# Kernel optimization log

Measured on AMD Instinct MI355X. Metric: run time of the kernel, lower is better.

The kernel has to match this reference:

```python
import jax, jax.numpy as jnp
import numpy as np

N = 8192        # n_nodes
NFEAT = 512
NHID = 256
AVG_DEG = 32
K = 64          # mean_kwargs k
TEMP = 1.0      # mean_kwargs temperature


def setup_inputs() -> dict:
    key = jax.random.key(0)
    ks = jax.random.split(key, 5)
    x = jax.random.normal(ks[0], (N, NFEAT), jnp.float32)
    edge_index = jax.random.randint(ks[1], (2, N * AVG_DEG), 0, N, dtype=jnp.int64)
    W1 = jax.random.normal(ks[2], (NFEAT, NHID), jnp.float32) / np.sqrt(NFEAT)
    b1 = jnp.zeros((NHID,), jnp.float32)
    W2 = jax.random.normal(ks[3], (NHID, NHID), jnp.float32) / np.sqrt(NHID)
    b2 = jnp.zeros((NHID,), jnp.float32)
    return {"x": x, "edge_index": edge_index, "W1": W1, "b1": b1, "W2": W2, "b2": b2}


def _gcn_norm(edge_index, n, dtype):
    # PyG gcn_norm: add self-loops (weight 1), deg over col, sym normalization
    loops = jnp.arange(n, dtype=edge_index.dtype)
    row = jnp.concatenate([edge_index[0], loops])
    col = jnp.concatenate([edge_index[1], loops])
    w = jnp.ones(row.shape[0], dtype)
    deg = jnp.zeros((n,), dtype).at[col].add(w)
    dis = jnp.where(deg > 0, jax.lax.rsqrt(jnp.where(deg > 0, deg, 1.0)), 0.0)
    return row, col, dis[row] * w * dis[col]


def _soft_k_medoid(row, col, w, x):
    # soft_weighted_medoid_k_neighborhood(A, x, k=K, temperature=TEMP, with_weight_correction=True)
    n, d = x.shape
    A = jnp.zeros((n, n), x.dtype).at[row, col].add(w)   # coalesced dense adjacency
    topk_a, topk_idx = jax.lax.top_k(A, K)               # [n, K] neighbor weights / ids
    xk = x[topk_idx]                                     # [n, K, d]
    sq = jnp.sum(xk * xk, axis=-1)                       # [n, K]
    G = jnp.einsum('nkd,nld->nkl', xk, xk)               # Gram per node
    d2 = jnp.maximum(sq[:, :, None] + sq[:, None, :] - 2.0 * G, 0.0)
    pos = d2 > 0
    dist = jnp.where(pos, jnp.sqrt(jnp.where(pos, d2, 1.0)), 0.0)  # safe sqrt (grad-safe)
    # weighted sum of distances to each top-k candidate j: c[n,j] = sum_l a[n,l] * ||x_l - x_j||
    c = jnp.einsum('nl,nlj->nj', topk_a, dist)
    c = jnp.where(topk_a == 0, jnp.finfo(x.dtype).max, c)
    soft = jax.nn.softmax(-c / TEMP, axis=-1)            # [n, K]
    soft = soft * topk_a                                 # with_weight_correction
    soft = soft / jnp.sum(soft, axis=-1, keepdims=True)
    row_sum = jnp.sum(A, axis=-1)                        # preserve neighborhood mass
    return row_sum[:, None] * jnp.einsum('nk,nkd->nd', soft, xk)


def reference(x, edge_index, W1, b1, W2, b2):
    n = x.shape[0]
    row, col, w = _gcn_norm(edge_index, n, x.dtype)
    h = jax.nn.relu(_soft_k_medoid(row, col, w, x @ W1) + b1)   # gc1 + relu (dropout: eval = identity)
    return jax.nn.relu(_soft_k_medoid(row, col, w, h @ W2) + b2)  # gc2 + relu
```

## Files before the change

kernel.cpp:

```cpp
#include <hip/hip_runtime.h>

typedef _Float16 half4 __attribute__((ext_vector_type(4)));
typedef _Float16 half8 __attribute__((ext_vector_type(8)));
typedef float f32x4 __attribute__((ext_vector_type(4)));

#define NNODE 8192
#define NHID  256
#define RCAP  128
#define KCAP  64

__global__ __launch_bounds__(256) void k_fused1(
    int* deg, int* rowcnt, int* flag, const void* edges,
    const float* __restrict__ W1, _Float16* __restrict__ w1T,
    const float* __restrict__ W2, _Float16* __restrict__ w2T) {
    const int b = blockIdx.x, t = threadIdx.x;
    if (b < 32) {
        int i = b * 256 + t;
        deg[i] = 0; rowcnt[i] = 0;
        if (i == 0) {
            const long long* e = (const long long*)edges;
            int ok = 1;
            for (int k = 0; k < 64; ++k) { long long v = e[k]; if (v < 0 || v >= NNODE) ok = 0; }
            *flag = ok;
        }
    } else if (b < 32 + 512) {
        int idx = (b - 32) * 256 + t;
        int k = idx >> 8, n = idx & 255;
        w1T[(size_t)n * 512 + k] = (_Float16)W1[idx];
    } else {
        int idx = (b - 544) * 256 + t;
        int k = idx >> 8, n = idx & 255;
        w2T[(size_t)n * 256 + k] = (_Float16)W2[idx];
    }
}

#define GLS 72

__device__ __forceinline__ void gemm_body(
    const float* __restrict__ Af32, const _Float16* __restrict__ Ahi,
    const _Float16* __restrict__ BT, _Float16* __restrict__ Chi,
    int K, int af32, int bm, int bn) {
    __shared__ _Float16 sA[64][GLS];
    __shared__ _Float16 sB[64][GLS];
    const int t = threadIdx.x;
    const int lane = t & 63, L15 = lane & 15, q = lane >> 4;
    const int w = t >> 6, wr = w >> 1, wc = w & 1;
    f32x4 acc[2][2];
#pragma unroll
    for (int a = 0; a < 2; ++a)
#pragma unroll
        for (int b2 = 0; b2 < 2; ++b2) acc[a][b2] = (f32x4){0.f, 0.f, 0.f, 0.f};

    for (int k0 = 0; k0 < K; k0 += 64) {
        if (af32) {
#pragma unroll
            for (int i = 0; i < 4; ++i) {
                int row = i * 16 + (t >> 4), kc = (t & 15) * 4;
                float4 v = *(const float4*)(Af32 + (size_t)(bm + row) * K + k0 + kc);
                half4 h;
                h[0] = (_Float16)v.x; h[1] = (_Float16)v.y;
                h[2] = (_Float16)v.z; h[3] = (_Float16)v.w;
                *(half4*)&sA[row][kc] = h;
            }
        } else {
#pragma unroll
            for (int i = 0; i < 2; ++i) {
                int row = i * 32 + (t >> 3), ch = t & 7;
                *(half8*)&sA[row][ch * 8] =
                    *(const half8*)(Ahi + (size_t)(bm + row) * K + k0 + ch * 8);
            }
        }
#pragma unroll
        for (int i = 0; i < 2; ++i) {
            int row = i * 32 + (t >> 3), ch = t & 7;
            *(half8*)&sB[row][ch * 8] =
                *(const half8*)(BT + (size_t)(bn + row) * K + k0 + ch * 8);
        }
        __syncthreads();
#pragma unroll
        for (int ks = 0; ks < 2; ++ks) {
            const int ko = ks * 32 + q * 8;
            half8 ah[2], bh[2];
#pragma unroll
            for (int tr = 0; tr < 2; ++tr)
                ah[tr] = *(const half8*)&sA[32 * wr + 16 * tr + L15][ko];
#pragma unroll
            for (int tc = 0; tc < 2; ++tc)
                bh[tc] = *(const half8*)&sB[32 * wc + 16 * tc + L15][ko];
#pragma unroll
            for (int tr = 0; tr < 2; ++tr)
#pragma unroll
                for (int tc = 0; tc < 2; ++tc)
                    acc[tr][tc] = __builtin_amdgcn_mfma_f32_16x16x32_f16(ah[tr], bh[tc], acc[tr][tc], 0, 0, 0);
        }
        __syncthreads();
    }
#pragma unroll
    for (int tr = 0; tr < 2; ++tr)
#pragma unroll
        for (int tc = 0; tc < 2; ++tc)
#pragma unroll
            for (int r = 0; r < 4; ++r) {
                int rowg = bm + 32 * wr + 16 * tr + q * 4 + r;
                int colg = bn + 32 * wc + 16 * tc + L15;
                Chi[(size_t)rowg * NHID + colg] = (_Float16)acc[tr][tc][r];
            }
}

__global__ __launch_bounds__(256) void k_fused2(
    const void* edges, const int* flag, int* rowcnt, int* nbr, int* deg, int E, int nbuild,
    const float* __restrict__ x, const _Float16* __restrict__ w1T, _Float16* __restrict__ X1) {
    if ((int)blockIdx.x < nbuild) {
        int i = blockIdx.x * 256 + threadIdx.x;
        int total = E + NNODE;
        if (i >= total) return;
        int r, c;
        if (i < E) {
            if (*flag) {
                const long long* e = (const long long*)edges;
                r = (int)e[i]; c = (int)e[E + i];
            } else {
                const int* e = (const int*)edges;
                r = e[i]; c = e[E + i];
            }
        } else { r = i - E; c = r; }
        int pos = atomicAdd(&rowcnt[r], 1);
        if (pos < RCAP) nbr[r * RCAP + pos] = c;
        atomicAdd(&deg[c], 1);
    } else {
        int g = blockIdx.x - nbuild;
        gemm_body(x, nullptr, w1T, X1, 512, 1, (g >> 2) * 64, (g & 3) * 64);
    }
}

__global__ __launch_bounds__(256) void k_gemm(
    const _Float16* __restrict__ Ahi, const _Float16* __restrict__ BT,
    _Float16* __restrict__ Chi, int K) {
    gemm_body(nullptr, Ahi, BT, Chi, K, 0, blockIdx.x * 64, blockIdx.y * 64);
}

__global__ __launch_bounds__(256) void k_dedup(const int* __restrict__ nbr,
                                               const int* __restrict__ rowcnt,
                                               const int* __restrict__ deg,
                                               int* __restrict__ cols,
                                               float* __restrict__ wout,
                                               float* __restrict__ rsum) {
    __shared__ int lc[2][RCAP];
    __shared__ float lw[2][RCAP];
    __shared__ unsigned char kp[2][RCAP];
    __shared__ int s_cw[2][2];
    __shared__ float s_rw[2][2];
    const int t = threadIdx.x;
    const int half = t >> 7, st = t & 127;
    const int wid = st >> 6, lane = t & 63;
    const int r = blockIdx.x * 2 + half;
    int n = rowcnt[r]; if (n > RCAP) n = RCAP;
    if (st < n) lc[half][st] = nbr[r * RCAP + st];
    __syncthreads();
    float dr = 1.f / sqrtf((float)deg[r]);
    bool keep = false; float wv = 0.f;
    if (st < n) {
        int c = lc[half][st];
        int mult = 0; bool first = true;
        for (int i = 0; i < n; ++i) {
            int ci = lc[half][i];
            if (ci == c) { mult++; if (i < st) first = false; }
        }
        keep = first;
        if (first) wv = (float)mult * dr * (1.f / sqrtf((float)deg[c]));
    }
    kp[half][st] = keep ? 1 : 0; lw[half][st] = wv;
    float rv = wv;
#pragma unroll
    for (int d = 1; d < 64; d <<= 1) rv += __shfl_xor(rv, d, 64);
    unsigned long long b = __ballot(keep);
    int pre = __popcll(b & ((1ull << lane) - 1ull));
    int cw = __popcll(b);
    if (lane == 0) { s_cw[half][wid] = cw; s_rw[half][wid] = rv; }
    __syncthreads();
    int total = s_cw[half][0] + s_cw[half][1];
    if (st == 0) rsum[r] = s_rw[half][0] + s_rw[half][1];
    const int base = r * KCAP;
    if (total <= KCAP) {
        int off = (wid ? s_cw[half][0] : 0) + pre;
        if (keep) { cols[base + off] = lc[half][st]; wout[base + off] = wv; }
        for (int m = total + st; m < KCAP; m += 128) { cols[base + m] = r; wout[base + m] = 0.f; }
    } else if (st == 0) {
        for (int s = 0; s < KCAP; ++s) {
            int best = -1;
            for (int i = 0; i < n; ++i) {
                if (!kp[half][i]) continue;
                if (best < 0 || lw[half][i] > lw[half][best] ||
                    (lw[half][i] == lw[half][best] && lc[half][i] < lc[half][best])) best = i;
            }
            cols[base + s] = lc[half][best]; wout[base + s] = lw[half][best]; kp[half][best] = 0;
        }
    }
}

#define MS 264

__global__ __launch_bounds__(256, 4) void k_medoid(
    const _Float16* __restrict__ Xhi,
    const float* __restrict__ bias,
    float* __restrict__ OutF, _Float16* __restrict__ OutHi,
    const int* __restrict__ cols, const float* __restrict__ wts,
    const float* __restrict__ rsum, int writeH) {
    __shared__ _Float16 sh[64][MS];
    __shared__ float s_a[64];
    __shared__ float s_sq[64];
    __shared__ float s_cpart[2][64];
    __shared__ float s_u[64];
    __shared__ int   s_cols[64];
    __shared__ float s_red[4][288];

    const int node = blockIdx.x;
    const int t = threadIdx.x;
    const int w = t >> 6, lane = t & 63;
    const int L15 = lane & 15, q = lane >> 4;
    const int wr = w >> 1, wc = w & 1;

    if (t < 64) { s_cols[t] = cols[node * KCAP + t]; s_a[t] = wts[node * KCAP + t]; }
    __syncthreads();

    {
        const int ch = t & 31, rr = t >> 5;
        float ps[8];
#pragma unroll
        for (int i = 0; i < 8; ++i) {
            int l = i * 8 + rr;
            half8 v = *(const half8*)(Xhi + ((size_t)s_cols[l] << 8) + ch * 8);
            *(half8*)&sh[l][ch * 8] = v;
            float s = 0.f;
#pragma unroll
            for (int e = 0; e < 8; ++e) { float f = (float)v[e]; s = fmaf(f, f, s); }
            ps[i] = s;
        }
#pragma unroll
        for (int d = 1; d < 32; d <<= 1)
#pragma unroll
            for (int i = 0; i < 8; ++i) ps[i] += __shfl_xor(ps[i], d, 64);
        if (ch == 0) {
#pragma unroll
            for (int i = 0; i < 8; ++i) s_sq[i * 8 + rr] = ps[i];
        }
    }
    __syncthreads();

    f32x4 acc[2][2];
#pragma unroll
    for (int a = 0; a < 2; ++a)
#pragma unroll
        for (int b = 0; b < 2; ++b) acc[a][b] = (f32x4){0.f, 0.f, 0.f, 0.f};
#pragma unroll
    for (int ks = 0; ks < 8; ++ks) {
        const int ko = ks * 32 + q * 8;
        half8 ah[2], bh[2];
#pragma unroll
        for (int tr = 0; tr < 2; ++tr) ah[tr] = *(const half8*)&sh[32 * wr + 16 * tr + L15][ko];
#pragma unroll
        for (int tc = 0; tc < 2; ++tc) bh[tc] = *(const half8*)&sh[32 * wc + 16 * tc + L15][ko];
#pragma unroll
        for (int tr = 0; tr < 2; ++tr)
#pragma unroll
            for (int tc = 0; tc < 2; ++tc)
                acc[tr][tc] = __builtin_amdgcn_mfma_f32_16x16x32_f16(ah[tr], bh[tc], acc[tr][tc], 0, 0, 0);
    }

#pragma unroll
    for (int tc = 0; tc < 2; ++tc) {
        const int colg = 32 * wc + 16 * tc + L15;
        const float sqc = s_sq[colg];
        float pj = 0.f;
#pragma unroll
        for (int tr = 0; tr < 2; ++tr)
#pragma unroll
            for (int r = 0; r < 4; ++r) {
                int rowg = 32 * wr + 16 * tr + q * 4 + r;
                float d2 = s_sq[rowg] + sqc - 2.f * acc[tr][tc][r];
                float dist = d2 > 0.f ? __builtin_amdgcn_sqrtf(d2) : 0.f;
                pj = fmaf(s_a[rowg], dist, pj);
            }
        pj += __shfl_xor(pj, 16, 64);
        pj += __shfl_xor(pj, 32, 64);
        if (q == 0) s_cpart[wr][colg] = pj;
    }
    __syncthreads();

    if (w == 0) {
        int j = lane;
        float c = s_cpart[0][j] + s_cpart[1][j];
        float aj = s_a[j];
        bool valid = aj > 0.f;
        float cv = valid ? c : 3.4e38f;
        float mn = cv;
#pragma unroll
        for (int d = 1; d < 64; d <<= 1) mn = fminf(mn, __shfl_xor(mn, d, 64));
        float e = valid ? __expf(mn - c) * aj : 0.f;
        float s = e;
#pragma unroll
        for (int d = 1; d < 64; d <<= 1) s += __shfl_xor(s, d, 64);
        s_u[j] = e * (rsum[node] / s);
    }
    __syncthreads();

    const int oct = t & 31, jb = t >> 5;
    float accd[8] = {0.f, 0.f, 0.f, 0.f, 0.f, 0.f, 0.f, 0.f};
#pragma unroll
    for (int jj = 0; jj < 8; ++jj) {
        int j = jb * 8 + jj;
        float u = s_u[j];
        half8 xv = *(const half8*)&sh[j][8 * oct];
#pragma unroll
        for (int e = 0; e < 8; ++e) accd[e] = fmaf(u, (float)xv[e], accd[e]);
    }
#pragma unroll
    for (int e = 0; e < 8; ++e) accd[e] += __shfl_xor(accd[e], 32, 64);
    if (lane < 32) {
#pragma unroll
        for (int e = 0; e < 8; ++e) s_red[w][9 * oct + e] = accd[e];
    }
    __syncthreads();
    const int idx = 9 * (t >> 3) + (t & 7);
    float o = s_red[0][idx] + s_red[1][idx] + s_red[2][idx] + s_red[3][idx];
    float res = fmaxf(o + bias[t], 0.f);
    size_t oi = (size_t)node * NHID + t;
    if (writeH) OutHi[oi] = (_Float16)res;
    else        OutF[oi] = res;
}

extern "C" void kernel_launch(void* const* d_in, const int* in_sizes, int n_in,
                              void* d_out, int out_size, void* d_ws, size_t ws_size,
                              hipStream_t stream) {
    const float* x  = (const float*)d_in[0];
    const void*  ei = d_in[1];
    const float* W1 = (const float*)d_in[2];
    const float* b1 = (const float*)d_in[3];
    const float* W2 = (const float*)d_in[4];
    const float* b2 = (const float*)d_in[5];
    float* out = (float*)d_out;
    const int E = in_sizes[1] / 2;

    char* p = (char*)d_ws;
    auto alloc = [&](size_t bytes) { char* q = p; p += (bytes + 255) & ~(size_t)255; return q; };
    int*      deg    = (int*)alloc((size_t)NNODE * 4);
    int*      rowcnt = (int*)alloc((size_t)NNODE * 4);
    int*      flag   = (int*)alloc(256);
    int*      colsA  = (int*)alloc((size_t)NNODE * KCAP * 4);
    float*    wA     = (float*)alloc((size_t)NNODE * KCAP * 4);
    float*    rsum   = (float*)alloc((size_t)NNODE * 4);
    _Float16* w1T    = (_Float16*)alloc((size_t)512 * NHID * 2);
    _Float16* w2T    = (_Float16*)alloc((size_t)NHID * NHID * 2);
    _Float16* X1hi   = (_Float16*)alloc((size_t)NNODE * NHID * 2);
    _Float16* Hhi    = (_Float16*)alloc((size_t)NNODE * NHID * 2);
    int*      nbr    = (int*)alloc((size_t)NNODE * RCAP * 4);

    const int nbuild = (E + NNODE + 255) / 256;

    k_fused1<<<32 + 512 + 256, 256, 0, stream>>>(deg, rowcnt, flag, ei, W1, w1T, W2, w2T);
    k_fused2<<<nbuild + 512, 256, 0, stream>>>(ei, flag, rowcnt, nbr, deg, E, nbuild, x, w1T, X1hi);
    k_dedup<<<NNODE / 2, 256, 0, stream>>>(nbr, rowcnt, deg, colsA, wA, rsum);
    k_medoid<<<NNODE, 256, 0, stream>>>(X1hi, b1, nullptr, Hhi, colsA, wA, rsum, 1);
    k_gemm<<<dim3(NNODE / 64, NHID / 64), 256, 0, stream>>>(Hhi, w2T, X1hi, 256);
    k_medoid<<<NNODE, 256, 0, stream>>>(X1hi, b2, out, nullptr, colsA, wA, rsum, 0);
}
```

Baseline: 240.0 us.

## Add half-size medoid path for nodes with at most 32 neighbors

k_dedup now records each row's deduplicated neighbor count. k_medoid uses it to branch: rows with 32 or fewer neighbors gather only 32 feature rows, compute a single 32x32 Gram tile (one MFMA tile per wave), and skip the padded rows in the final weighted sum. Both paths now take squared norms from the Gram diagonal, replacing the separate sum-of-squares shuffle reduction. This cuts gather traffic and MFMA work for the roughly half of nodes below the threshold, at the cost of a divergent, more complex kernel and higher register pressure.

Result: faster. 218.4 us (-9.0%).

```diff
diff --git a/kernel.cpp b/kernel.cpp
--- a/kernel.cpp
+++ b/kernel.cpp
@@ -144,7 +144,8 @@
                                                const int* __restrict__ deg,
                                                int* __restrict__ cols,
                                                float* __restrict__ wout,
-                                               float* __restrict__ rsum) {
+                                               float* __restrict__ rsum,
+                                               int* __restrict__ ncnt) {
     __shared__ int lc[2][RCAP];
     __shared__ float lw[2][RCAP];
     __shared__ unsigned char kp[2][RCAP];
@@ -179,7 +180,7 @@
     if (lane == 0) { s_cw[half][wid] = cw; s_rw[half][wid] = rv; }
     __syncthreads();
     int total = s_cw[half][0] + s_cw[half][1];
-    if (st == 0) rsum[r] = s_rw[half][0] + s_rw[half][1];
+    if (st == 0) { rsum[r] = s_rw[half][0] + s_rw[half][1]; ncnt[r] = total; }
     const int base = r * KCAP;
     if (total <= KCAP) {
         int off = (wid ? s_cw[half][0] : 0) + pre;
@@ -205,7 +206,7 @@
     const float* __restrict__ bias,
     float* __restrict__ OutF, _Float16* __restrict__ OutHi,
     const int* __restrict__ cols, const float* __restrict__ wts,
-    const float* __restrict__ rsum, int writeH) {
+    const float* __restrict__ rsum, const int* __restrict__ ncnt, int writeH) {
     __shared__ _Float16 sh[64][MS];
     __shared__ float s_a[64];
     __shared__ float s_sq[64];
@@ -219,71 +220,110 @@
     const int w = t >> 6, lane = t & 63;
     const int L15 = lane & 15, q = lane >> 4;
     const int wr = w >> 1, wc = w & 1;
+    const bool small = (ncnt[node] <= 32);
 
     if (t < 64) { s_cols[t] = cols[node * KCAP + t]; s_a[t] = wts[node * KCAP + t]; }
     __syncthreads();
 
     {
         const int ch = t & 31, rr = t >> 5;
-        float ps[8];
-#pragma unroll
-        for (int i = 0; i < 8; ++i) {
-            int l = i * 8 + rr;
-            half8 v = *(const half8*)(Xhi + ((size_t)s_cols[l] << 8) + ch * 8);
-            *(half8*)&sh[l][ch * 8] = v;
-            float s = 0.f;
-#pragma unroll
-            for (int e = 0; e < 8; ++e) { float f = (float)v[e]; s = fmaf(f, f, s); }
-            ps[i] = s;
-        }
-#pragma unroll
-        for (int d = 1; d < 32; d <<= 1)
-#pragma unroll
-            for (int i = 0; i < 8; ++i) ps[i] += __shfl_xor(ps[i], d, 64);
-        if (ch == 0) {
-#pragma unroll
-            for (int i = 0; i < 8; ++i) s_sq[i * 8 + rr] = ps[i];
-        }
-    }
-    __syncthreads();
-
-    f32x4 acc[2][2];
-#pragma unroll
-    for (int a = 0; a < 2; ++a)
-#pragma unroll
-        for (int b = 0; b < 2; ++b) acc[a][b] = (f32x4){0.f, 0.f, 0.f, 0.f};
-#pragma unroll
-    for (int ks = 0; ks < 8; ++ks) {
-        const int ko = ks * 32 + q * 8;
-        half8 ah[2], bh[2];
-#pragma unroll
-        for (int tr = 0; tr < 2; ++tr) ah[tr] = *(const half8*)&sh[32 * wr + 16 * tr + L15][ko];
-#pragma unroll
-        for (int tc = 0; tc < 2; ++tc) bh[tc] = *(const half8*)&sh[32 * wc + 16 * tc + L15][ko];
-#pragma unroll
-        for (int tr = 0; tr < 2; ++tr)
-#pragma unroll
-            for (int tc = 0; tc < 2; ++tc)
-                acc[tr][tc] = __builtin_amdgcn_mfma_f32_16x16x32_f16(ah[tr], bh[tc], acc[tr][tc], 0, 0, 0);
-    }
-
-#pragma unroll
-    for (int tc = 0; tc < 2; ++tc) {
-        const int colg = 32 * wc + 16 * tc + L15;
-        const float sqc = s_sq[colg];
+        if (small) {
+#pragma unroll
+            for (int i = 0; i < 4; ++i) {
+                int l = i * 8 + rr;
+                *(half8*)&sh[l][ch * 8] = *(const half8*)(Xhi + ((size_t)s_cols[l] << 8) + ch * 8);
+            }
+        } else {
+#pragma unroll
+            for (int i = 0; i < 8; ++i) {
+                int l = i * 8 + rr;
+                *(half8*)&sh[l][ch * 8] = *(const half8*)(Xhi + ((size_t)s_cols[l] << 8) + ch * 8);
+            }
+        }
+    }
+    __syncthreads();
+
+    if (small) {
+        f32x4 acc = (f32x4){0.f, 0.f, 0.f, 0.f};
+#pragma unroll
+        for (int ks = 0; ks < 8; ++ks) {
+            const int ko = ks * 32 + q * 8;
+            half8 ah = *(const half8*)&sh[16 * wr + L15][ko];
+            half8 bh = *(const half8*)&sh[16 * wc + L15][ko];
+            acc = __builtin_amdgcn_mfma_f32_16x16x32_f16(ah, bh, acc, 0, 0, 0);
+        }
+        if (wr == wc) {
+#pragma unroll
+            for (int r = 0; r < 4; ++r)
+                if (L15 == q * 4 + r) s_sq[16 * wr + L15] = acc[r];
+        }
+        __syncthreads();
+        f32x4 sq4 = *(const f32x4*)&s_sq[16 * wr + 4 * q];
+        f32x4 a4  = *(const f32x4*)&s_a [16 * wr + 4 * q];
+        const float sqc = s_sq[16 * wc + L15];
         float pj = 0.f;
 #pragma unroll
-        for (int tr = 0; tr < 2; ++tr)
-#pragma unroll
-            for (int r = 0; r < 4; ++r) {
-                int rowg = 32 * wr + 16 * tr + q * 4 + r;
-                float d2 = s_sq[rowg] + sqc - 2.f * acc[tr][tc][r];
-                float dist = d2 > 0.f ? __builtin_amdgcn_sqrtf(d2) : 0.f;
-                pj = fmaf(s_a[rowg], dist, pj);
-            }
+        for (int r = 0; r < 4; ++r) {
+            float d2 = sq4[r] + sqc - 2.f * acc[r];
+            float dist = d2 > 0.f ? __builtin_amdgcn_sqrtf(d2) : 0.f;
+            pj = fmaf(a4[r], dist, pj);
+        }
         pj += __shfl_xor(pj, 16, 64);
         pj += __shfl_xor(pj, 32, 64);
-        if (q == 0) s_cpart[wr][colg] = pj;
+        if (q == 0) s_cpart[wr][16 * wc + L15] = pj;
+    } else {
+        f32x4 acc[2][2];
+#pragma unroll
+        for (int a = 0; a < 2; ++a)
+#pragma unroll
+            for (int b = 0; b < 2; ++b) acc[a][b] = (f32x4){0.f, 0.f, 0.f, 0.f};
+#pragma unroll
+        for (int ks = 0; ks < 8; ++ks) {
+            const int ko = ks * 32 + q * 8;
+            half8 ah[2], bh[2];
+#pragma unroll
+            for (int tr = 0; tr < 2; ++tr) ah[tr] = *(const half8*)&sh[32 * wr + 16 * tr + L15][ko];
+#pragma unroll
+            for (int tc = 0; tc < 2; ++tc) bh[tc] = *(const half8*)&sh[32 * wc + 16 * tc + L15][ko];
+#pragma unroll
+            for (int tr = 0; tr < 2; ++tr)
+#pragma unroll
+                for (int tc = 0; tc < 2; ++tc)
+                    acc[tr][tc] = __builtin_amdgcn_mfma_f32_16x16x32_f16(ah[tr], bh[tc], acc[tr][tc], 0, 0, 0);
+        }
+#pragma unroll
+        for (int tr = 0; tr < 2; ++tr)
+#pragma unroll
+            for (int tc = 0; tc < 2; ++tc)
+                if (32 * wr + 16 * tr == 32 * wc + 16 * tc) {
+#pragma unroll
+                    for (int r = 0; r < 4; ++r)
+                        if (L15 == q * 4 + r) s_sq[32 * wr + 16 * tr + L15] = acc[tr][tc][r];
+                }
+        __syncthreads();
+        f32x4 sq4[2], a4[2];
+#pragma unroll
+        for (int tr = 0; tr < 2; ++tr) {
+            sq4[tr] = *(const f32x4*)&s_sq[32 * wr + 16 * tr + 4 * q];
+            a4[tr]  = *(const f32x4*)&s_a [32 * wr + 16 * tr + 4 * q];
+        }
+#pragma unroll
+        for (int tc = 0; tc < 2; ++tc) {
+            const int colg = 32 * wc + 16 * tc + L15;
+            const float sqc = s_sq[colg];
+            float pj = 0.f;
+#pragma unroll
+            for (int tr = 0; tr < 2; ++tr)
+#pragma unroll
+                for (int r = 0; r < 4; ++r) {
+                    float d2 = sq4[tr][r] + sqc - 2.f * acc[tr][tc][r];
+                    float dist = d2 > 0.f ? __builtin_amdgcn_sqrtf(d2) : 0.f;
+                    pj = fmaf(a4[tr][r], dist, pj);
+                }
+            pj += __shfl_xor(pj, 16, 64);
+            pj += __shfl_xor(pj, 32, 64);
+            if (q == 0) s_cpart[wr][colg] = pj;
+        }
     }
     __syncthreads();
 
@@ -306,13 +346,15 @@
 
     const int oct = t & 31, jb = t >> 5;
     float accd[8] = {0.f, 0.f, 0.f, 0.f, 0.f, 0.f, 0.f, 0.f};
-#pragma unroll
-    for (int jj = 0; jj < 8; ++jj) {
-        int j = jb * 8 + jj;
-        float u = s_u[j];
-        half8 xv = *(const half8*)&sh[j][8 * oct];
-#pragma unroll
-        for (int e = 0; e < 8; ++e) accd[e] = fmaf(u, (float)xv[e], accd[e]);
+    if (!small || jb < 4) {
+#pragma unroll
+        for (int jj = 0; jj < 8; ++jj) {
+            int j = jb * 8 + jj;
+            float u = s_u[j];
+            half8 xv = *(const half8*)&sh[j][8 * oct];
+#pragma unroll
+            for (int e = 0; e < 8; ++e) accd[e] = fmaf(u, (float)xv[e], accd[e]);
+        }
     }
 #pragma unroll
     for (int e = 0; e < 8; ++e) accd[e] += __shfl_xor(accd[e], 32, 64);
@@ -349,6 +391,7 @@
     int*      colsA  = (int*)alloc((size_t)NNODE * KCAP * 4);
     float*    wA     = (float*)alloc((size_t)NNODE * KCAP * 4);
     float*    rsum   = (float*)alloc((size_t)NNODE * 4);
+    int*      ncnt   = (int*)alloc((size_t)NNODE * 4);
     _Float16* w1T    = (_Float16*)alloc((size_t)512 * NHID * 2);
     _Float16* w2T    = (_Float16*)alloc((size_t)NHID * NHID * 2);
     _Float16* X1hi   = (_Float16*)alloc((size_t)NNODE * NHID * 2);
@@ -359,8 +402,8 @@
 
     k_fused1<<<32 + 512 + 256, 256, 0, stream>>>(deg, rowcnt, flag, ei, W1, w1T, W2, w2T);
     k_fused2<<<nbuild + 512, 256, 0, stream>>>(ei, flag, rowcnt, nbr, deg, E, nbuild, x, w1T, X1hi);
-    k_dedup<<<NNODE / 2, 256, 0, stream>>>(nbr, rowcnt, deg, colsA, wA, rsum);
-    k_medoid<<<NNODE, 256, 0, stream>>>(X1hi, b1, nullptr, Hhi, colsA, wA, rsum, 1);
+    k_dedup<<<NNODE / 2, 256, 0, stream>>>(nbr, rowcnt, deg, colsA, wA, rsum, ncnt);
+    k_medoid<<<NNODE, 256, 0, stream>>>(X1hi, b1, nullptr, Hhi, colsA, wA, rsum, ncnt, 1);
     k_gemm<<<dim3(NNODE / 64, NHID / 64), 256, 0, stream>>>(Hhi, w2T, X1hi, 256);
-    k_medoid<<<NNODE, 256, 0, stream>>>(X1hi, b2, out, nullptr, colsA, wA, rsum, 0);
-}
+    k_medoid<<<NNODE, 256, 0, stream>>>(X1hi, b2, out, nullptr, colsA, wA, rsum, ncnt, 0);
+}
```

## Halve medoid shared tile via two-phase Gram, precast x to fp16

Applied to the files above, without the earlier changes.

The medoid kernel now stages the 64 gathered neighbor rows in two 128-column halves, so its LDS tile is half the size and launch bounds allow 6 blocks per CU instead of 4. Squared norms are read off the Gram diagonal instead of a separate shuffle reduction. The final weighted sum re-reads the first half of each row from global memory because only the second half is still in LDS. Separately, x is converted to fp16 in a dedicated pass in the first kernel, so the first GEMM loads fp16 tiles directly. This costs an extra global round trip of x and extra gathered reads in the medoid kernel.

Result: faster. 214.6 us (-10.6%).

```diff
diff --git a/kernel.cpp b/kernel.cpp
--- a/kernel.cpp
+++ b/kernel.cpp
@@ -12,7 +12,8 @@
 __global__ __launch_bounds__(256) void k_fused1(
     int* deg, int* rowcnt, int* flag, const void* edges,
     const float* __restrict__ W1, _Float16* __restrict__ w1T,
-    const float* __restrict__ W2, _Float16* __restrict__ w2T) {
+    const float* __restrict__ W2, _Float16* __restrict__ w2T,
+    const float* __restrict__ x, _Float16* __restrict__ xh) {
     const int b = blockIdx.x, t = threadIdx.x;
     if (b < 32) {
         int i = b * 256 + t;
@@ -23,12 +24,19 @@
             for (int k = 0; k < 64; ++k) { long long v = e[k]; if (v < 0 || v >= NNODE) ok = 0; }
             *flag = ok;
         }
-    } else if (b < 32 + 512) {
-        int idx = (b - 32) * 256 + t;
+    } else if (b < 32 + 4096) {
+        int i = (b - 32) * 256 + t;
+        float4 v = ((const float4*)x)[i];
+        half4 h;
+        h[0] = (_Float16)v.x; h[1] = (_Float16)v.y;
+        h[2] = (_Float16)v.z; h[3] = (_Float16)v.w;
+        *(half4*)&xh[4 * (size_t)i] = h;
+    } else if (b < 32 + 4096 + 512) {
+        int idx = (b - 4128) * 256 + t;
         int k = idx >> 8, n = idx & 255;
         w1T[(size_t)n * 512 + k] = (_Float16)W1[idx];
     } else {
-        int idx = (b - 544) * 256 + t;
+        int idx = (b - 4640) * 256 + t;
         int k = idx >> 8, n = idx & 255;
         w2T[(size_t)n * 256 + k] = (_Float16)W2[idx];
     }
@@ -37,9 +45,8 @@
 #define GLS 72
 
 __device__ __forceinline__ void gemm_body(
-    const float* __restrict__ Af32, const _Float16* __restrict__ Ahi,
-    const _Float16* __restrict__ BT, _Float16* __restrict__ Chi,
-    int K, int af32, int bm, int bn) {
+    const _Float16* __restrict__ Ahi, const _Float16* __restrict__ BT,
+    _Float16* __restrict__ Chi, int K, int bm, int bn) {
     __shared__ _Float16 sA[64][GLS];
     __shared__ _Float16 sB[64][GLS];
     const int t = threadIdx.x;
@@ -52,27 +59,11 @@
         for (int b2 = 0; b2 < 2; ++b2) acc[a][b2] = (f32x4){0.f, 0.f, 0.f, 0.f};
 
     for (int k0 = 0; k0 < K; k0 += 64) {
-        if (af32) {
-#pragma unroll
-            for (int i = 0; i < 4; ++i) {
-                int row = i * 16 + (t >> 4), kc = (t & 15) * 4;
-                float4 v = *(const float4*)(Af32 + (size_t)(bm + row) * K + k0 + kc);
-                half4 h;
-                h[0] = (_Float16)v.x; h[1] = (_Float16)v.y;
-                h[2] = (_Float16)v.z; h[3] = (_Float16)v.w;
-                *(half4*)&sA[row][kc] = h;
-            }
-        } else {
-#pragma unroll
-            for (int i = 0; i < 2; ++i) {
-                int row = i * 32 + (t >> 3), ch = t & 7;
-                *(half8*)&sA[row][ch * 8] =
-                    *(const half8*)(Ahi + (size_t)(bm + row) * K + k0 + ch * 8);
-            }
-        }
 #pragma unroll
         for (int i = 0; i < 2; ++i) {
             int row = i * 32 + (t >> 3), ch = t & 7;
+            *(half8*)&sA[row][ch * 8] =
+                *(const half8*)(Ahi + (size_t)(bm + row) * K + k0 + ch * 8);
             *(half8*)&sB[row][ch * 8] =
                 *(const half8*)(BT + (size_t)(bn + row) * K + k0 + ch * 8);
         }
@@ -109,7 +100,7 @@
 
 __global__ __launch_bounds__(256) void k_fused2(
     const void* edges, const int* flag, int* rowcnt, int* nbr, int* deg, int E, int nbuild,
-    const float* __restrict__ x, const _Float16* __restrict__ w1T, _Float16* __restrict__ X1) {
+    const _Float16* __restrict__ xh, const _Float16* __restrict__ w1T, _Float16* __restrict__ X1) {
     if ((int)blockIdx.x < nbuild) {
         int i = blockIdx.x * 256 + threadIdx.x;
         int total = E + NNODE;
@@ -129,14 +120,14 @@
         atomicAdd(&deg[c], 1);
     } else {
         int g = blockIdx.x - nbuild;
-        gemm_body(x, nullptr, w1T, X1, 512, 1, (g >> 2) * 64, (g & 3) * 64);
+        gemm_body(xh, w1T, X1, 512, (g >> 2) * 64, (g & 3) * 64);
     }
 }
 
 __global__ __launch_bounds__(256) void k_gemm(
     const _Float16* __restrict__ Ahi, const _Float16* __restrict__ BT,
     _Float16* __restrict__ Chi, int K) {
-    gemm_body(nullptr, Ahi, BT, Chi, K, 0, blockIdx.x * 64, blockIdx.y * 64);
+    gemm_body(Ahi, BT, Chi, K, blockIdx.x * 64, blockIdx.y * 64);
 }
 
 __global__ __launch_bounds__(256) void k_dedup(const int* __restrict__ nbr,
@@ -198,15 +189,15 @@
     }
 }
 
-#define MS 264
-
-__global__ __launch_bounds__(256, 4) void k_medoid(
+#define SK 136
+
+__global__ __launch_bounds__(256, 6) void k_medoid(
     const _Float16* __restrict__ Xhi,
     const float* __restrict__ bias,
     float* __restrict__ OutF, _Float16* __restrict__ OutHi,
     const int* __restrict__ cols, const float* __restrict__ wts,
     const float* __restrict__ rsum, int writeH) {
-    __shared__ _Float16 sh[64][MS];
+    __shared__ _Float16 sh[64][SK];
     __shared__ float s_a[64];
     __shared__ float s_sq[64];
     __shared__ float s_cpart[2][64];
@@ -223,50 +214,55 @@
     if (t < 64) { s_cols[t] = cols[node * KCAP + t]; s_a[t] = wts[node * KCAP + t]; }
     __syncthreads();
 
-    {
-        const int ch = t & 31, rr = t >> 5;
-        float ps[8];
-#pragma unroll
-        for (int i = 0; i < 8; ++i) {
-            int l = i * 8 + rr;
-            half8 v = *(const half8*)(Xhi + ((size_t)s_cols[l] << 8) + ch * 8);
-            *(half8*)&sh[l][ch * 8] = v;
-            float s = 0.f;
-#pragma unroll
-            for (int e = 0; e < 8; ++e) { float f = (float)v[e]; s = fmaf(f, f, s); }
-            ps[i] = s;
-        }
-#pragma unroll
-        for (int d = 1; d < 32; d <<= 1)
-#pragma unroll
-            for (int i = 0; i < 8; ++i) ps[i] += __shfl_xor(ps[i], d, 64);
-        if (ch == 0) {
-#pragma unroll
-            for (int i = 0; i < 8; ++i) s_sq[i * 8 + rr] = ps[i];
-        }
-    }
-    __syncthreads();
-
     f32x4 acc[2][2];
 #pragma unroll
     for (int a = 0; a < 2; ++a)
 #pragma unroll
         for (int b = 0; b < 2; ++b) acc[a][b] = (f32x4){0.f, 0.f, 0.f, 0.f};
-#pragma unroll
-    for (int ks = 0; ks < 8; ++ks) {
-        const int ko = ks * 32 + q * 8;
-        half8 ah[2], bh[2];
-#pragma unroll
-        for (int tr = 0; tr < 2; ++tr) ah[tr] = *(const half8*)&sh[32 * wr + 16 * tr + L15][ko];
-#pragma unroll
-        for (int tc = 0; tc < 2; ++tc) bh[tc] = *(const half8*)&sh[32 * wc + 16 * tc + L15][ko];
-#pragma unroll
-        for (int tr = 0; tr < 2; ++tr)
-#pragma unroll
-            for (int tc = 0; tc < 2; ++tc)
-                acc[tr][tc] = __builtin_amdgcn_mfma_f32_16x16x32_f16(ah[tr], bh[tc], acc[tr][tc], 0, 0, 0);
-    }
-
+
+    const int ch = t & 15, rr = t >> 4;
+    for (int phase = 0; phase < 2; ++phase) {
+#pragma unroll
+        for (int i = 0; i < 4; ++i) {
+            int l = i * 16 + rr;
+            *(half8*)&sh[l][ch * 8] =
+                *(const half8*)(Xhi + ((size_t)s_cols[l] << 8) + phase * 128 + ch * 8);
+        }
+        __syncthreads();
+#pragma unroll
+        for (int ks = 0; ks < 4; ++ks) {
+            const int ko = ks * 32 + q * 8;
+            half8 ah[2], bh[2];
+#pragma unroll
+            for (int tr = 0; tr < 2; ++tr) ah[tr] = *(const half8*)&sh[32 * wr + 16 * tr + L15][ko];
+#pragma unroll
+            for (int tc = 0; tc < 2; ++tc) bh[tc] = *(const half8*)&sh[32 * wc + 16 * tc + L15][ko];
+#pragma unroll
+            for (int tr = 0; tr < 2; ++tr)
+#pragma unroll
+                for (int tc = 0; tc < 2; ++tc)
+                    acc[tr][tc] = __builtin_amdgcn_mfma_f32_16x16x32_f16(ah[tr], bh[tc], acc[tr][tc], 0, 0, 0);
+        }
+        if (phase == 0) __syncthreads();
+    }
+
+#pragma unroll
+    for (int tr = 0; tr < 2; ++tr)
+#pragma unroll
+        for (int tc = 0; tc < 2; ++tc)
+            if (32 * wr + 16 * tr == 32 * wc + 16 * tc) {
+#pragma unroll
+                for (int r = 0; r < 4; ++r)
+                    if (L15 == q * 4 + r) s_sq[32 * wr + 16 * tr + L15] = acc[tr][tc][r];
+            }
+    __syncthreads();
+
+    f32x4 sq4[2], a4[2];
+#pragma unroll
+    for (int tr = 0; tr < 2; ++tr) {
+        sq4[tr] = *(const f32x4*)&s_sq[32 * wr + 16 * tr + 4 * q];
+        a4[tr]  = *(const f32x4*)&s_a [32 * wr + 16 * tr + 4 * q];
+    }
 #pragma unroll
     for (int tc = 0; tc < 2; ++tc) {
         const int colg = 32 * wc + 16 * tc + L15;
@@ -276,10 +272,9 @@
         for (int tr = 0; tr < 2; ++tr)
 #pragma unroll
             for (int r = 0; r < 4; ++r) {
-                int rowg = 32 * wr + 16 * tr + q * 4 + r;
-                float d2 = s_sq[rowg] + sqc - 2.f * acc[tr][tc][r];
+                float d2 = sq4[tr][r] + sqc - 2.f * acc[tr][tc][r];
                 float dist = d2 > 0.f ? __builtin_amdgcn_sqrtf(d2) : 0.f;
-                pj = fmaf(s_a[rowg], dist, pj);
+                pj = fmaf(a4[tr][r], dist, pj);
             }
         pj += __shfl_xor(pj, 16, 64);
         pj += __shfl_xor(pj, 32, 64);
@@ -310,7 +305,9 @@
     for (int jj = 0; jj < 8; ++jj) {
         int j = jb * 8 + jj;
         float u = s_u[j];
-        half8 xv = *(const half8*)&sh[j][8 * oct];
+        half8 xv;
+        if (oct < 16) xv = *(const half8*)(Xhi + ((size_t)s_cols[j] << 8) + oct * 8);
+        else          xv = *(const half8*)&sh[j][(oct - 16) * 8];
 #pragma unroll
         for (int e = 0; e < 8; ++e) accd[e] = fmaf(u, (float)xv[e], accd[e]);
     }
@@ -349,6 +346,7 @@
     int*      colsA  = (int*)alloc((size_t)NNODE * KCAP * 4);
     float*    wA     = (float*)alloc((size_t)NNODE * KCAP * 4);
     float*    rsum   = (float*)alloc((size_t)NNODE * 4);
+    _Float16* xh     = (_Float16*)alloc((size_t)NNODE * 512 * 2);
     _Float16* w1T    = (_Float16*)alloc((size_t)512 * NHID * 2);
     _Float16* w2T    = (_Float16*)alloc((size_t)NHID * NHID * 2);
     _Float16* X1hi   = (_Float16*)alloc((size_t)NNODE * NHID * 2);
@@ -357,8 +355,8 @@
 
     const int nbuild = (E + NNODE + 255) / 256;
 
-    k_fused1<<<32 + 512 + 256, 256, 0, stream>>>(deg, rowcnt, flag, ei, W1, w1T, W2, w2T);
-    k_fused2<<<nbuild + 512, 256, 0, stream>>>(ei, flag, rowcnt, nbr, deg, E, nbuild, x, w1T, X1hi);
+    k_fused1<<<32 + 4096 + 512 + 256, 256, 0, stream>>>(deg, rowcnt, flag, ei, W1, w1T, W2, w2T, x, xh);
+    k_fused2<<<nbuild + 512, 256, 0, stream>>>(ei, flag, rowcnt, nbr, deg, E, nbuild, xh, w1T, X1hi);
     k_dedup<<<NNODE / 2, 256, 0, stream>>>(nbr, rowcnt, deg, colsA, wA, rsum);
     k_medoid<<<NNODE, 256, 0, stream>>>(X1hi, b1, nullptr, Hhi, colsA, wA, rsum, 1);
     k_gemm<<<dim3(NNODE / 64, NHID / 64), 256, 0, stream>>>(Hhi, w2T, X1hi, 256);
```
